# Kernel tuning notes

Hardware: AMD Instinct MI355X
Metric: run time of the kernel (lower is better)

## Reference

```python
import jax, jax.numpy as jnp
import numpy as np

NUM_EXPERTS = 64
NOISE_STD = 1.0
CAPACITY = 32  # top-C items per expert (experts-choice routing)
D_MODEL = 512
NUM_GROUPS = 8
GROUP_SIZE = 2048


def _top_items_per_expert_dispatcher(gates):
    """Experts-choice dispatcher for one group.

    gates: (S, E) softmax gate values.
    Returns:
      dispatch: (E, C, S) one-hot selection of the top-C items per expert.
      combine:  (S, E, C) gate value if item s is expert e's c-th pick, else 0.
    """
    s = gates.shape[0]
    # Each expert picks its top-C items by gate value.
    _, top_idx = jax.lax.top_k(gates.T, CAPACITY)          # (E, C)
    dispatch = jax.nn.one_hot(top_idx, s, dtype=gates.dtype)  # (E, C, S)
    combine = jnp.einsum('se,ecs->sec', gates, dispatch)      # (S, E, C)
    return dispatch, combine


def setup_inputs() -> dict:
    key = jax.random.key(0)
    k1, k2 = jax.random.split(key)
    inputs = jax.random.normal(k1, (NUM_GROUPS, GROUP_SIZE, D_MODEL), dtype=jnp.float32)
    # Dense(num_experts, use_bias=False) kernel, lecun-normal-ish scale.
    W = jax.random.normal(k2, (D_MODEL, NUM_EXPERTS), dtype=jnp.float32) * (D_MODEL ** -0.5)
    return {"inputs": inputs, "W": W}


def reference(inputs, W):
    # Gating projection: (G, S, D) x (D, E) -> (G, S, E)
    logits = jnp.einsum('gsd,de->gse', inputs, W)
    # Noisy gating: noise_std scaled by 1/num_experts (as in the module).
    noise_scale = NOISE_STD / NUM_EXPERTS
    noise = noise_scale * jax.random.normal(jax.random.key(42), logits.shape, dtype=logits.dtype)
    gates = jax.nn.softmax(logits + noise, axis=-1)  # (G, S, E)
    # vmap the per-group top-items-per-expert dispatcher over groups.
    dispatch, combine = jax.vmap(_top_items_per_expert_dispatcher)(gates)
    return combine, dispatch
```

## Files before the change

### kernel.cpp

```cpp
#include <hip/hip_runtime.h>
#include <math.h>
#include <stdint.h>

#define NG 8
#define GS 2048
#define DM 512
#define NE 64
#define CAP 32
#define NROWS (NG * GS)
#define COMBINE_ELEMS (33554432ull)

#define GATE_BLOCKS 512
#define XSTc 68
#define CHW (32 * XSTc)
#define TBS 21

typedef float f32x4 __attribute__((ext_vector_type(4)));
typedef double f64x2 __attribute__((ext_vector_type(2)));
typedef double f64x4 __attribute__((ext_vector_type(4)));
typedef unsigned long long u64;

__device__ __forceinline__ void threefry2x32(uint32_t k0, uint32_t k1,
                                             uint32_t x0, uint32_t x1,
                                             uint32_t& o0, uint32_t& o1) {
  uint32_t ks[3] = {k0, k1, k0 ^ k1 ^ 0x1BD11BDAu};
  x0 += ks[0];
  x1 += ks[1];
  const uint32_t rot[2][4] = {{13u, 15u, 26u, 6u}, {17u, 29u, 16u, 24u}};
#pragma unroll
  for (int i = 0; i < 5; ++i) {
#pragma unroll
    for (int j = 0; j < 4; ++j) {
      uint32_t r = rot[i & 1][j];
      x0 += x1;
      x1 = (x1 << r) | (x1 >> (32u - r));
      x1 ^= x0;
    }
    x0 += ks[(i + 1) % 3];
    x1 += ks[(i + 2) % 3] + (uint32_t)(i + 1);
  }
  o0 = x0;
  o1 = x1;
}

__device__ __forceinline__ float erfinv_xla(float x) {
  float w = -log1pf(-x * x);
  float p;
  if (w < 5.0f) {
    w = w - 2.5f;
    p = 2.81022636e-08f;
    p = __fmaf_rn(p, w, 3.43273939e-07f);
    p = __fmaf_rn(p, w, -3.5233877e-06f);
    p = __fmaf_rn(p, w, -4.39150654e-06f);
    p = __fmaf_rn(p, w, 0.00021858087f);
    p = __fmaf_rn(p, w, -0.00125372503f);
    p = __fmaf_rn(p, w, -0.00417768164f);
    p = __fmaf_rn(p, w, 0.246640727f);
    p = __fmaf_rn(p, w, 1.50140941f);
  } else {
    w = sqrtf(w) - 3.0f;
    p = -0.000200214257f;
    p = __fmaf_rn(p, w, 0.000100950558f);
    p = __fmaf_rn(p, w, 0.00134934322f);
    p = __fmaf_rn(p, w, -0.00367342844f);
    p = __fmaf_rn(p, w, 0.00573950773f);
    p = __fmaf_rn(p, w, -0.0076224613f);
    p = __fmaf_rn(p, w, 0.00943887047f);
    p = __fmaf_rn(p, w, 1.00167406f);
    p = __fmaf_rn(p, w, 2.83297682f);
  }
  return p * x;
}

__device__ __forceinline__ float jax_normal(uint32_t idx) {
  uint32_t o0, o1;
  threefry2x32(0u, 42u, 0u, idx, o0, o1);
  uint32_t bits = o0 ^ o1;
  float f = __uint_as_float((bits >> 9) | 0x3f800000u) - 1.0f;
  const float lo = __uint_as_float(0xBF7FFFFFu);
  float v = fmaxf(lo, f * 2.0f + lo);
  return __uint_as_float(0x3FB504F3u) * erfinv_xla(v);
}

__global__ __launch_bounds__(256) void wprep_kernel(
    const float* __restrict__ Wt, double* __restrict__ Wd) {
  const int i = blockIdx.x * 256 + threadIdx.x;
  const int t = i & 3, i15 = (i >> 2) & 15, row = i >> 6;
  Wd[i] = (double)Wt[row * NE + t * 16 + i15];
}

__global__ __launch_bounds__(256) void gate_kernel(
    const float* __restrict__ x,
    const double* __restrict__ Wd,
    float* __restrict__ gatesT) {
  __shared__ float xs[2 * CHW];
  __shared__ double pd[128 * 16];
  const int gid = blockIdx.x;
  const int tid = threadIdx.x;
  const int l = tid & 63;
  const int w4 = tid >> 6;
  const int wr = w4 & 1;
  const int kh = w4 >> 1;
  const int row0b = gid * 32;
  const int row0 = row0b + wr * 16;

  const int i15 = l & 15;
  const int k4 = l >> 4;

  const int sr0 = tid >> 4, sc0 = (tid & 15) << 2;
  const int sr1 = (tid + 256) >> 4, sc1 = ((tid + 256) & 15) << 2;
  const float* xg0 = x + (size_t)(row0b + sr0) * DM + sc0;
  const float* xg1 = x + (size_t)(row0b + sr1) * DM + sc1;

  f32x4 a0[8], a1[8];
#pragma unroll
  for (int ck = 0; ck < 8; ++ck) {
    a0[ck] = *(const f32x4*)(xg0 + ck * 64);
    a1[ck] = *(const f32x4*)(xg1 + ck * 64);
  }

  f64x4 dr = {0., 0., 0., 0.};
  dr = __builtin_amdgcn_mfma_f64_16x16x4f64((double)i15, 0.25, dr, 0, 0, 0);
  int perm[4];
#pragma unroll
  for (int r = 0; r < 4; ++r) perm[r] = ((int)(dr[r] + 0.5)) & 15;

  *(f32x4*)(xs + sr0 * XSTc + sc0) = a0[0];
  *(f32x4*)(xs + sr1 * XSTc + sc1) = a1[0];
  __syncthreads();

  f64x4 acc[4] = {{0., 0., 0., 0.}, {0., 0., 0., 0.},
                  {0., 0., 0., 0.}, {0., 0., 0., 0.}};
  const int abase = (wr * 16 + i15) * XSTc + k4;
  const int kl0 = kh * 8;
#pragma unroll
  for (int ck = 0; ck < 8; ++ck) {
    const int cur = ck & 1;
    if (ck < 7) {
      *(f32x4*)(xs + (cur ^ 1) * CHW + sr0 * XSTc + sc0) = a0[ck + 1];
      *(f32x4*)(xs + (cur ^ 1) * CHW + sr1 * XSTc + sc1) = a1[ck + 1];
    }
    const float* ar = xs + cur * CHW + abase;
#pragma unroll
    for (int kkl = 0; kkl < 8; ++kkl) {
      const int kloc = kl0 + kkl;
      const double a = (double)ar[kloc * 4];
      const int kk = ck * 16 + kloc;
      const double* wrow = Wd + ((size_t)((kk << 2) + k4)) * 64 + i15 * 4;
      const f64x2 b01 = *(const f64x2*)(wrow + 0);
      const f64x2 b23 = *(const f64x2*)(wrow + 2);
      acc[0] = __builtin_amdgcn_mfma_f64_16x16x4f64(a, b01[0], acc[0], 0, 0, 0);
      acc[1] = __builtin_amdgcn_mfma_f64_16x16x4f64(a, b01[1], acc[1], 0, 0, 0);
      acc[2] = __builtin_amdgcn_mfma_f64_16x16x4f64(a, b23[0], acc[2], 0, 0, 0);
      acc[3] = __builtin_amdgcn_mfma_f64_16x16x4f64(a, b23[1], acc[3], 0, 0, 0);
    }
    __syncthreads();
  }

  if (kh == 1) {
    double* dst = pd + ((size_t)(wr * 64 + l)) * 16;
#pragma unroll
    for (int t = 0; t < 4; ++t)
#pragma unroll
      for (int r = 0; r < 4; ++r) dst[t * 4 + r] = acc[t][r];
  }
  __syncthreads();
  if (kh == 1) return;

  {
    const double* src = pd + ((size_t)(wr * 64 + l)) * 16;
#pragma unroll
    for (int t = 0; t < 4; ++t)
#pragma unroll
      for (int r = 0; r < 4; ++r) acc[t][r] += src[t * 4 + r];
  }

  float gatef[4][4];
#pragma unroll
  for (int r = 0; r < 4; ++r) {
    const int row = row0 + perm[r];
    double v[4];
    double m = -1.0e300;
#pragma unroll
    for (int t = 0; t < 4; ++t) {
      const float logit = (float)acc[t][r];
      const float noised =
          logit + 0.015625f * jax_normal((uint32_t)(row * NE + 16 * t + i15));
      v[t] = (double)noised;
      m = fmax(m, v[t]);
    }
#pragma unroll
    for (int off = 1; off < 16; off <<= 1) m = fmax(m, __shfl_xor(m, off, 64));
    double s = 0.0;
#pragma unroll
    for (int t = 0; t < 4; ++t) {
      v[t] = exp(v[t] - m);
      s += v[t];
    }
#pragma unroll
    for (int off = 1; off < 16; off <<= 1) s += __shfl_xor(s, off, 64);
#pragma unroll
    for (int t = 0; t < 4; ++t) gatef[t][r] = (float)(v[t] / s);
  }

  float* tb = xs + wr * (NE * TBS);
#pragma unroll
  for (int t = 0; t < 4; ++t)
#pragma unroll
    for (int r = 0; r < 4; ++r)
      tb[(16 * t + i15) * TBS + perm[r]] = gatef[t][r];

  const int g = row0 >> 11;
  const int s0 = row0 & (GS - 1);
  float* drow = gatesT + ((size_t)(g * NE + l)) * GS + s0;
#pragma unroll
  for (int c = 0; c < 4; ++c) {
    f32x4 o;
#pragma unroll
    for (int i = 0; i < 4; ++i) o[i] = tb[l * TBS + 4 * c + i];
    *(f32x4*)&drow[4 * c] = o;
  }
}

__global__ __launch_bounds__(256) void topwrite_kernel(
    const float* __restrict__ gatesT,
    float* __restrict__ out) {
  __shared__ u64 keys[CAP];
  __shared__ int sel_s[CAP];
  __shared__ float sel_v[CAP];
  __shared__ unsigned char c_of_s[GS];
  const int ge = blockIdx.x;
  const int g = ge >> 6, e = ge & 63;
  const int tid = threadIdx.x;
  const int lane = tid & 63, w = tid >> 6;

  ((u64*)c_of_s)[tid] = ~0ull;

  if (w == 0) {
    const float* base = gatesT + (size_t)ge * GS;
    u64 K[32];
#pragma unroll
    for (int k = 0; k < 8; ++k) {
      const f32x4 t = *(const f32x4*)(base + k * 256 + lane * 4);
#pragma unroll
      for (int i = 0; i < 4; ++i) {
        const int s = k * 256 + lane * 4 + i;
        K[k * 4 + i] = ((u64)__float_as_uint(t[i]) << 32) | (u64)(2047 - s);
      }
    }
#pragma unroll
    for (int k = 2; k <= 32; k <<= 1) {
#pragma unroll
      for (int d = k >> 1; d > 0; d >>= 1) {
#pragma unroll
        for (int j = 0; j < 32; ++j) {
          const int ixj = j ^ d;
          if (ixj > j) {
            const bool asc = ((j & k) == 0);
            const u64 a = K[j], b = K[ixj];
            const bool sw = asc ? (a > b) : (a < b);
            K[j] = sw ? b : a;
            K[ixj] = sw ? a : b;
          }
        }
      }
    }
#pragma unroll
    for (int m = 1; m < 64; m <<= 1) {
      u64 tmp[32];
#pragma unroll
      for (int j = 0; j < 32; ++j) tmp[j] = __shfl_xor(K[31 - j], m, 64);
#pragma unroll
      for (int j = 0; j < 32; ++j) K[j] = (K[j] > tmp[j]) ? K[j] : tmp[j];
#pragma unroll
      for (int d = 16; d > 0; d >>= 1) {
#pragma unroll
        for (int j = 0; j < 32; ++j) {
          if ((j & d) == 0) {
            const u64 a = K[j], b = K[j | d];
            const bool sw = (a > b);
            K[j] = sw ? b : a;
            K[j | d] = sw ? a : b;
          }
        }
      }
    }
#pragma unroll
    for (int c = 0; c < CAP; ++c) {
      if (lane == c) keys[c] = K[31 - c];
    }
  }
  __syncthreads();

  if (tid < CAP) {
    const u64 key = keys[tid];
    sel_s[tid] = 2047 - (int)(key & 0x7FFull);
    sel_v[tid] = __uint_as_float((uint32_t)(key >> 32));
  }
  __syncthreads();
  if (tid < CAP) c_of_s[sel_s[tid]] = (unsigned char)tid;
  __syncthreads();

  float* drow_base = out + COMBINE_ELEMS + (size_t)ge * CAP * GS;
#pragma unroll
  for (int rr = 0; rr < 8; ++rr) {
    const int c = 8 * w + rr;
    const int sc = sel_s[c];
    float* rowp = drow_base + (size_t)c * GS;
#pragma unroll
    for (int j = 0; j < 8; ++j) {
      const int pos = j * 256 + lane * 4;
      f32x4 v;
      v[0] = (sc == pos + 0) ? 1.0f : 0.0f;
      v[1] = (sc == pos + 1) ? 1.0f : 0.0f;
      v[2] = (sc == pos + 2) ? 1.0f : 0.0f;
      v[3] = (sc == pos + 3) ? 1.0f : 0.0f;
      *(f32x4*)&rowp[pos] = v;
    }
  }

  const int pos = (lane & 7) * 4;
  for (int it = 0; it < 64; ++it) {
    const int s = 512 * w + 8 * it + (lane >> 3);
    const int c = c_of_s[s];
    const float val = (c != 255) ? sel_v[c & 31] : 0.0f;
    const int d = c - pos;
    f32x4 v;
    v[0] = (d == 0) ? val : 0.0f;
    v[1] = (d == 1) ? val : 0.0f;
    v[2] = (d == 2) ? val : 0.0f;
    v[3] = (d == 3) ? val : 0.0f;
    *(f32x4*)&out[(((size_t)(g * GS + s)) * NE + e) * CAP + pos] = v;
  }
}

extern "C" void kernel_launch(void* const* d_in, const int* in_sizes, int n_in,
                              void* d_out, int out_size, void* d_ws,
                              size_t ws_size, hipStream_t stream) {
  (void)in_sizes; (void)n_in; (void)ws_size; (void)out_size;
  const float* x = (const float*)d_in[0];
  const float* Wt = (const float*)d_in[1];
  float* out = (float*)d_out;
  float* gatesT = (float*)d_ws;
  double* Wd = (double*)((char*)d_ws + ((size_t)NROWS * NE * 4));

  wprep_kernel<<<128, 256, 0, stream>>>(Wt, Wd);
  gate_kernel<<<GATE_BLOCKS, 256, 0, stream>>>(x, Wd, gatesT);
  topwrite_kernel<<<NG * NE, 256, 0, stream>>>(gatesT, out);
}
```

Measured before the change: 123.0 us.

## Split gate kernel into 16-row blocks with 4-way K split per block

Each gate block now handles 16 rows instead of 32, so twice as many blocks are launched. The four waves split the K dimension four ways instead of two-by-two over rows and K, with three partial sums reduced through shared memory. The up-front register prefetch of all x chunks is replaced by loading one chunk per iteration, issued before the MFMA work and stored to the other LDS buffer after it. This aims for more parallelism and lower register pressure, at the cost of a larger cross-wave reduction, more blocks re-reading W, and less prefetch depth.

New measurement: 121.1 us. About the same (-1.6%).

```diff
diff --git a/kernel.cpp b/kernel.cpp
--- a/kernel.cpp
+++ b/kernel.cpp
@@ -10,10 +10,10 @@
 #define NROWS (NG * GS)
 #define COMBINE_ELEMS (33554432ull)
 
-#define GATE_BLOCKS 512
+#define GATE_BLOCKS 1024
 #define XSTc 68
-#define CHW (32 * XSTc)
-#define TBS 21
+#define CHW (16 * XSTc)
+#define TBS 17
 
 typedef float f32x4 __attribute__((ext_vector_type(4)));
 typedef double f64x2 __attribute__((ext_vector_type(2)));
@@ -94,30 +94,15 @@
     const double* __restrict__ Wd,
     float* __restrict__ gatesT) {
   __shared__ float xs[2 * CHW];
-  __shared__ double pd[128 * 16];
+  __shared__ double pd[3 * 64 * 16];
   const int gid = blockIdx.x;
   const int tid = threadIdx.x;
   const int l = tid & 63;
-  const int w4 = tid >> 6;
-  const int wr = w4 & 1;
-  const int kh = w4 >> 1;
-  const int row0b = gid * 32;
-  const int row0 = row0b + wr * 16;
+  const int kh = tid >> 6;
+  const int row0 = gid * 16;
 
   const int i15 = l & 15;
   const int k4 = l >> 4;
-
-  const int sr0 = tid >> 4, sc0 = (tid & 15) << 2;
-  const int sr1 = (tid + 256) >> 4, sc1 = ((tid + 256) & 15) << 2;
-  const float* xg0 = x + (size_t)(row0b + sr0) * DM + sc0;
-  const float* xg1 = x + (size_t)(row0b + sr1) * DM + sc1;
-
-  f32x4 a0[8], a1[8];
-#pragma unroll
-  for (int ck = 0; ck < 8; ++ck) {
-    a0[ck] = *(const f32x4*)(xg0 + ck * 64);
-    a1[ck] = *(const f32x4*)(xg1 + ck * 64);
-  }
 
   f64x4 dr = {0., 0., 0., 0.};
   dr = __builtin_amdgcn_mfma_f64_16x16x4f64((double)i15, 0.25, dr, 0, 0, 0);
@@ -125,24 +110,25 @@
 #pragma unroll
   for (int r = 0; r < 4; ++r) perm[r] = ((int)(dr[r] + 0.5)) & 15;
 
-  *(f32x4*)(xs + sr0 * XSTc + sc0) = a0[0];
-  *(f32x4*)(xs + sr1 * XSTc + sc1) = a1[0];
+  const int sr = tid >> 4, sc = (tid & 15) << 2;
+  const float* xg = x + (size_t)(row0 + sr) * DM + sc;
+  float* xl = xs + sr * XSTc + sc;
+
+  *(f32x4*)xl = *(const f32x4*)xg;
   __syncthreads();
 
   f64x4 acc[4] = {{0., 0., 0., 0.}, {0., 0., 0., 0.},
                   {0., 0., 0., 0.}, {0., 0., 0., 0.}};
-  const int abase = (wr * 16 + i15) * XSTc + k4;
-  const int kl0 = kh * 8;
-#pragma unroll
+  const int abase = i15 * XSTc + k4;
+  const int kl0 = kh * 4;
   for (int ck = 0; ck < 8; ++ck) {
     const int cur = ck & 1;
-    if (ck < 7) {
-      *(f32x4*)(xs + (cur ^ 1) * CHW + sr0 * XSTc + sc0) = a0[ck + 1];
-      *(f32x4*)(xs + (cur ^ 1) * CHW + sr1 * XSTc + sc1) = a1[ck + 1];
-    }
+    f32x4 a0;
+    const bool more = (ck < 7);
+    if (more) a0 = *(const f32x4*)(xg + (ck + 1) * 64);
     const float* ar = xs + cur * CHW + abase;
 #pragma unroll
-    for (int kkl = 0; kkl < 8; ++kkl) {
+    for (int kkl = 0; kkl < 4; ++kkl) {
       const int kloc = kl0 + kkl;
       const double a = (double)ar[kloc * 4];
       const int kk = ck * 16 + kloc;
@@ -154,21 +140,23 @@
       acc[2] = __builtin_amdgcn_mfma_f64_16x16x4f64(a, b23[0], acc[2], 0, 0, 0);
       acc[3] = __builtin_amdgcn_mfma_f64_16x16x4f64(a, b23[1], acc[3], 0, 0, 0);
     }
+    if (more) *(f32x4*)(xs + (cur ^ 1) * CHW + sr * XSTc + sc) = a0;
     __syncthreads();
   }
 
-  if (kh == 1) {
-    double* dst = pd + ((size_t)(wr * 64 + l)) * 16;
+  if (kh != 0) {
+    double* dst = pd + ((size_t)((kh - 1) * 64 + l)) * 16;
 #pragma unroll
     for (int t = 0; t < 4; ++t)
 #pragma unroll
       for (int r = 0; r < 4; ++r) dst[t * 4 + r] = acc[t][r];
   }
   __syncthreads();
-  if (kh == 1) return;
-
-  {
-    const double* src = pd + ((size_t)(wr * 64 + l)) * 16;
+  if (kh != 0) return;
+
+#pragma unroll
+  for (int q = 0; q < 3; ++q) {
+    const double* src = pd + ((size_t)(q * 64 + l)) * 16;
 #pragma unroll
     for (int t = 0; t < 4; ++t)
 #pragma unroll
@@ -203,7 +191,7 @@
     for (int t = 0; t < 4; ++t) gatef[t][r] = (float)(v[t] / s);
   }
 
-  float* tb = xs + wr * (NE * TBS);
+  float* tb = xs;
 #pragma unroll
   for (int t = 0; t < 4; ++t)
 #pragma unroll
```
